# Kernel tuning notes

Measured on AMD Instinct MI355X. Metric: run time of the kernel, lower is better.

The kernel has to match this reference:

```python
import jax, jax.numpy as jnp
import numpy as np

NUM_CLASSES = 3
DICE_W, FOCAL_W, CONTR_W = 1.0, 1.0, 0.1
GAMMA, ALPHA = 2.0, 0.25
TEMP = 0.1
SCALE_WEIGHTS = (1.0, 0.8, 0.6)
SMOOTH = 1e-5


def setup_inputs() -> dict:
    key = jax.random.key(0)
    ks = jax.random.split(key, 7)
    return {
        "pred_maps": jax.random.normal(ks[0], (2, 3, 128, 128, 128), jnp.float32),
        "target": jax.random.randint(ks[1], (2, 128, 128, 128), 0, 3, jnp.int64),
        "fmap0": jax.random.normal(ks[2], (2, 48, 16, 16, 16), jnp.float32),
        "fmap1": jax.random.normal(ks[3], (2, 48, 8, 8, 8), jnp.float32),
        "fmap2": jax.random.normal(ks[4], (2, 48, 4, 4, 4), jnp.float32),
        "logits": jax.random.normal(ks[5], (2, 3), jnp.float32),
        "labels": jax.random.randint(ks[6], (2, 3), 0, 2, jnp.int32),
    }


def _dice_loss(pred, target):
    p = jax.nn.softmax(pred, axis=1)                      # [B,C,H,W,D]
    t = jnp.where(target == -1, 0, target)
    oh = jax.nn.one_hot(t, NUM_CLASSES, axis=1, dtype=p.dtype)  # [B,C,H,W,D]
    inter = (p * oh).sum((2, 3, 4))                       # [B,C]
    union = p.sum((2, 3, 4)) + oh.sum((2, 3, 4))
    dice = (2.0 * inter + SMOOTH) / (union + SMOOTH)      # [B,C]
    return 1.0 - dice[:, 1:].mean()                       # exclude background


def _focal_loss(logits, labels):
    pt = jax.nn.sigmoid(logits)
    pt = jnp.where(labels == 1, pt, 1.0 - pt)
    return (-ALPHA * (1.0 - pt) ** GAMMA * jnp.log(pt + 1e-6)).mean()


def _pair_loss(E, wa, wb, offdiag, positive):
    # E: [B,N,N] exp(sim/T); wa, wb: [B,N] class indicator weights
    W = wa[:, :, None] * wb[:, None, :]
    if offdiag is not None:
        W = W * offdiag
    cnt = W.sum((1, 2))
    mean = (E * W).sum((1, 2)) / jnp.maximum(cnt, 1.0)
    val = -jnp.log(mean + 1e-6) if positive else jnp.log1p(mean)
    return jnp.where(cnt > 0, val, 0.0)                   # [B]


def _scale_loss(feat, mask):
    B, C = feat.shape[:2]
    f = feat.reshape(B, C, -1)                            # [B,C,N]
    norm = jnp.sqrt((f * f).sum(1, keepdims=True))
    f = f / jnp.maximum(norm, 1e-12)                      # F.normalize(dim=1)
    m = mask.reshape(B, -1)                               # [B,N]
    E = jnp.exp(jnp.einsum('bcn,bcm->bnm', f, f) / TEMP)  # [B,N,N]
    N = m.shape[1]
    off = 1.0 - jnp.eye(N, dtype=f.dtype)
    w0 = (m == 0).astype(f.dtype)
    w1 = (m == 1).astype(f.dtype)
    w2 = (m == 2).astype(f.dtype)
    loss = _pair_loss(E, w1, w1, off, True)               # htx positive
    loss += _pair_loss(E, w2, w2, off, True)              # mh positive
    loss += _pair_loss(E, w1, w2, None, False)            # htx vs mh
    loss += _pair_loss(E, w0, w1, None, False)            # bg vs htx
    loss += _pair_loss(E, w0, w2, None, False)            # bg vs mh
    return loss.mean()                                    # batch_loss / B


def _contrastive_loss(fmaps, target):
    H = target.shape[1]
    total = 0.0
    for feat, w in zip(fmaps, SCALE_WEIGHTS):
        s = H // feat.shape[2]                            # exact nearest-downsample stride
        mask = target[:, ::s, ::s, ::s]
        total += w * _scale_loss(feat, mask)
    return total


def reference(pred_maps, target, fmap0, fmap1, fmap2, logits, labels):
    dice = _dice_loss(pred_maps, target)
    focal = _focal_loss(logits, labels)
    contr = _contrastive_loss((fmap0, fmap1, fmap2), target)
    total = DICE_W * dice + FOCAL_W * focal + CONTR_W * contr
    return (total, dice, focal, contr)
```

## Files before the change

kernel.cpp:

```cpp
#include <hip/hip_runtime.h>
#include <math.h>

#define VOX (128*128*128)
#define NCH 48

typedef _Float16 half8 __attribute__((ext_vector_type(8)));
typedef float floatx4 __attribute__((ext_vector_type(4)));

__device__ __forceinline__ float waveSum(float v) {
#pragma unroll
    for (int off = 32; off > 0; off >>= 1) v += __shfl_down(v, off, 64);
    return v;
}


__device__ __forceinline__ int elem_class(const int* __restrict__ target,
                                          int scale, int b, int n) {
    const int d = (scale == 0) ? 16 : (scale == 1) ? 8 : 4;
    const int s = 128 / d;
    int i3 = n % d, i2 = (n / d) % d, i1 = n / (d * d);
    return target[(size_t)b * VOX + (size_t)(i1 * s) * 16384 + (i2 * s) * 128 + (i3 * s)];
}

__global__ __launch_bounds__(256) void count_kernel(const int* __restrict__ target,
                                                    int* __restrict__ count_stage) {
    const int scale = blockIdx.y, b = blockIdx.z, z = scale * 2 + b, bx = blockIdx.x;
    const int N    = (scale == 0) ? 4096 : (scale == 1) ? 512 : 64;
    const int Npad = (scale == 0) ? 4096 : (scale == 1) ? 512 : 128;
    const int n = bx * 256 + threadIdx.x;
    int myK = -1;
    if (n < N)          myK = elem_class(target, scale, b, n);
    else if (n < Npad)  myK = 3;

    __shared__ int wc[4][4];
    const int lane = threadIdx.x & 63, w = threadIdx.x >> 6;
#pragma unroll
    for (int k = 0; k < 4; k++) {
        unsigned long long mb = __ballot(myK == k);
        if (lane == 0) wc[w][k] = (int)__popcll(mb);
    }
    __syncthreads();
    if (threadIdx.x < 4)
        count_stage[(z * 16 + bx) * 4 + threadIdx.x] =
            wc[0][threadIdx.x] + wc[1][threadIdx.x] + wc[2][threadIdx.x] + wc[3][threadIdx.x];
}

__global__ __launch_bounds__(256) void norm_scatter(const float* __restrict__ f0in,
                                                    const float* __restrict__ f1in,
                                                    const float* __restrict__ f2in,
                                                    const int* __restrict__ target,
                                                    _Float16* __restrict__ Fh0,
                                                    _Float16* __restrict__ Fh1,
                                                    _Float16* __restrict__ Fh2,
                                                    const int* __restrict__ count_stage) {
    const int scale = blockIdx.y, b = blockIdx.z, z = scale * 2 + b, bx = blockIdx.x;
    const int N    = (scale == 0) ? 4096 : (scale == 1) ? 512 : 64;
    const int Npad = (scale == 0) ? 4096 : (scale == 1) ? 512 : 128;
    if (bx * 256 >= Npad) return;
    const int tid = threadIdx.x, lane = tid & 63, w = tid >> 6;
    const int n = bx * 256 + tid;

    __shared__ int cs[64];
    __shared__ int wcls[4][4];
    if (tid < 64) cs[tid] = count_stage[z * 64 + tid];

    int myK = -1;
    if (n < N)         myK = elem_class(target, scale, b, n);
    else if (n < Npad) myK = 3;

    const unsigned long long below = (lane == 63) ? ~0ull >> 1 : (1ull << lane) - 1ull;
    int laneRank = 0;
#pragma unroll
    for (int k = 0; k < 4; k++) {
        unsigned long long mb = __ballot(myK == k);
        if (lane == 0) wcls[w][k] = (int)__popcll(mb);
        if (myK == k) laneRank = (int)__popcll(mb & below);
    }
    __syncthreads();
    if (myK < 0) return;

    int total[4];
#pragma unroll
    for (int k = 0; k < 4; k++) {
        int s = 0;
        for (int r = 0; r < 16; r++) s += cs[r * 4 + k];
        total[k] = s;
    }
    int dest = laneRank;
    for (int k = 0; k < myK; k++) dest += total[k];
    for (int r = 0; r < bx; r++) dest += cs[r * 4 + myK];
    for (int ww = 0; ww < w; ww++) dest += wcls[ww][myK];

    float v[NCH];
    float inv = 0.0f;
    if (n < N) {
        const float* fi = ((scale == 0) ? f0in : (scale == 1) ? f1in : f2in)
                          + (size_t)b * NCH * N + n;
        float ss = 0.0f;
#pragma unroll
        for (int c = 0; c < NCH; c++) { v[c] = fi[(size_t)c * N]; ss += v[c] * v[c]; }
        inv = 1.0f / fmaxf(sqrtf(ss), 1e-12f);
    } else {
#pragma unroll
        for (int c = 0; c < NCH; c++) v[c] = 0.0f;
    }
    _Float16* fo = ((scale == 0) ? Fh0 : (scale == 1) ? Fh1 : Fh2)
                   + (size_t)b * Npad * 64 + (size_t)dest * 64;
#pragma unroll
    for (int g = 0; g < 8; g++) {
        half8 h;
#pragma unroll
        for (int e = 0; e < 8; e++) {
            int c = g * 8 + e;
            h[e] = (c < NCH) ? (_Float16)(v[c] * inv) : (_Float16)0.0f;
        }
        *(half8*)(fo + g * 8) = h;
    }
}

__global__ __launch_bounds__(256) void dice_pair(const float* __restrict__ pred,
                                                 const int* __restrict__ target,
                                                 const _Float16* __restrict__ Fh0,
                                                 const _Float16* __restrict__ Fh1,
                                                 const _Float16* __restrict__ Fh2,
                                                 const int* __restrict__ count_stage,
                                                 float* __restrict__ dice_stage,
                                                 float* __restrict__ pair_stage) {
    const int bid = blockIdx.x;
    const int tid = threadIdx.x, lane = tid & 63, w = tid >> 6;
    __shared__ float red[4][6];

    if (bid >= 550) {
        const int local = bid - 550;
        const int b = local >> 9, bx = local & 511;
        const float4* p0 = (const float4*)(pred + (size_t)b * 3 * VOX);
        const float4* p1 = (const float4*)(pred + (size_t)b * 3 * VOX + VOX);
        const float4* p2 = (const float4*)(pred + (size_t)b * 3 * VOX + 2 * VOX);
        const int4*   tg = (const int4*)(target + (size_t)b * VOX);

        float vals[6] = {0, 0, 0, 0, 0, 0};
        const int V4 = VOX / 4;
        for (int v = bx * 256 + tid; v < V4; v += 512 * 256) {
            float4 a = p0[v], bq = p1[v], cq = p2[v];
            int4 t = tg[v];
            float xs[4][3] = {{a.x, bq.x, cq.x}, {a.y, bq.y, cq.y},
                              {a.z, bq.z, cq.z}, {a.w, bq.w, cq.w}};
            int ts[4] = {t.x, t.y, t.z, t.w};
#pragma unroll
            for (int e = 0; e < 4; e++) {
                float e0 = __expf(xs[e][0]), e1 = __expf(xs[e][1]), e2 = __expf(xs[e][2]);
                float inv = 1.0f / (e0 + e1 + e2);
                float q1 = e1 * inv, q2 = e2 * inv;
                vals[2] += q1;
                vals[3] += q2;
                int tt = ts[e];
                vals[0] += (tt == 1) ? q1 : 0.0f;
                vals[1] += (tt == 2) ? q2 : 0.0f;
                vals[4] += (tt == 1) ? 1.0f : 0.0f;
                vals[5] += (tt == 2) ? 1.0f : 0.0f;
            }
        }
#pragma unroll
        for (int k = 0; k < 6; k++) {
            float s = waveSum(vals[k]);
            if (lane == 0) red[w][k] = s;
        }
        __syncthreads();
        if (tid < 6) {
            float s = red[0][tid] + red[1][tid] + red[2][tid] + red[3][tid];
            dice_stage[(size_t)local * 8 + tid] = s;
        }
        return;
    }

    int z, t0, nt, tstep;
    if (bid < 528)      { z = bid / 264; t0 = bid % 264; nt = 2; tstep = 264; }
    else if (bid < 548) { int i = bid - 528; z = 2 + i / 10; t0 = i % 10; nt = 1; tstep = 0; }
    else                { z = 4 + (bid - 548); t0 = 0; nt = 1; tstep = 0; }

    const int scale = z >> 1, b = z & 1;
    const int Npad = (scale == 0) ? 4096 : (scale == 1) ? 512 : 128;
    const _Float16* F = ((scale == 0) ? Fh0 : (scale == 1) ? Fh1 : Fh2)
                        + (size_t)b * Npad * 64;
    int B1 = 0, B2 = 0, B3 = 0;
    for (int r = 0; r < 16; r++) {
        B1 += count_stage[(z * 16 + r) * 4 + 0];
        B2 += count_stage[(z * 16 + r) * 4 + 1];
        B3 += count_stage[(z * 16 + r) * 4 + 2];
    }
    B2 += B1; B3 += B2;

    const int wi = w >> 1, wj = w & 1;
    const int m = lane & 15, q = lane >> 4;

    float s[5] = {0, 0, 0, 0, 0};

    for (int it = 0; it < nt; it++) {
        int t = t0 + it * tstep;
        int by = (int)((sqrtf(8.0f * (float)t + 1.0f) - 1.0f) * 0.5f);
        while ((by + 1) * (by + 2) / 2 <= t) by++;
        while (by * (by + 1) / 2 > t) by--;
        int bx = t - by * (by + 1) / 2;

        const int ib = bx * 128 + wi * 64, jb = by * 128 + wj * 64;

        const bool diag = (ib == jb);
        const bool below = (ib > jb);
        int ciL = (ib >= B1) + (ib >= B2) + (ib >= B3);
        int ciH = (ib + 63 >= B1) + (ib + 63 >= B2) + (ib + 63 >= B3);
        int cjL = (jb >= B1) + (jb >= B2) + (jb >= B3);
        int cjH = (jb + 63 >= B1) + (jb + 63 >= B2) + (jb + 63 >= B3);
        const bool pure = (ciL == ciH) && (cjL == cjH) && !diag;
        int bucket = -1;
        float mult = 1.0f;
        if (pure) {
            int ci = ciL, cj = cjL;
            if (ci == 1 && cj == 1) { bucket = 0; mult = 2.0f; }
            else if (ci == 2 && cj == 2) { bucket = 1; mult = 2.0f; }
            else if (ci == 1 && cj == 2) bucket = 2;
            else if (ci == 0 && cj == 1) bucket = 3;
            else if (ci == 0 && cj == 2) bucket = 4;
        }
        if (below || (pure && bucket < 0)) continue;

        const _Float16* Ai = F + (size_t)(ib + m) * 64 + q * 8;
        const _Float16* Bj = F + (size_t)(jb + m) * 64 + q * 8;

        floatx4 acc_[4][4] = {};
#pragma unroll
        for (int k = 0; k < 2; k++) {
            half8 aF[4], bF[4];
#pragma unroll
            for (int t4 = 0; t4 < 4; t4++) {
                aF[t4] = *(const half8*)(Ai + t4 * 16 * 64 + k * 32);
                bF[t4] = *(const half8*)(Bj + t4 * 16 * 64 + k * 32);
            }
#pragma unroll
            for (int ti = 0; ti < 4; ti++)
#pragma unroll
                for (int tj = 0; tj < 4; tj++)
                    acc_[ti][tj] = __builtin_amdgcn_mfma_f32_16x16x32_f16(
                        aF[ti], bF[tj], acc_[ti][tj], 0, 0, 0);
        }

        if (pure) {
            float ps[4] = {0, 0, 0, 0};
#pragma unroll
            for (int ti = 0; ti < 4; ti++)
#pragma unroll
                for (int tj = 0; tj < 4; tj++)
#pragma unroll
                    for (int r = 0; r < 4; r++)
                        ps[r] += __expf(acc_[ti][tj][r] * 10.0f);
            s[bucket] += ((ps[0] + ps[1]) + (ps[2] + ps[3])) * mult;
        } else {
#pragma unroll
            for (int ti = 0; ti < 4; ti++) {
#pragma unroll
                for (int tj = 0; tj < 4; tj++) {
#pragma unroll
                    for (int r = 0; r < 4; r++) {
                        int gi = ib + ti * 16 + q * 4 + r;
                        int gj = jb + tj * 16 + m;
                        float e = __expf(acc_[ti][tj][r] * 10.0f);
                        bool ok = !diag || (gi < gj);
                        int ci = (gi >= B1) + (gi >= B2) + (gi >= B3);
                        int cj = (gj >= B1) + (gj >= B2) + (gj >= B3);
                        s[0] += (ok && ci == 1 && cj == 1) ? e + e : 0.0f;
                        s[1] += (ok && ci == 2 && cj == 2) ? e + e : 0.0f;
                        s[2] += (ok && ci == 1 && cj == 2) ? e : 0.0f;
                        s[3] += (ok && ci == 0 && cj == 1) ? e : 0.0f;
                        s[4] += (ok && ci == 0 && cj == 2) ? e : 0.0f;
                    }
                }
            }
        }
    }

#pragma unroll
    for (int k = 0; k < 5; k++) {
        float r = waveSum(s[k]);
        if (lane == 0) red[w][k] = r;
    }
    __syncthreads();
    if (tid < 5) {
        float r = red[0][tid] + red[1][tid] + red[2][tid] + red[3][tid];
        pair_stage[(size_t)bid * 8 + tid] = r;
    }
}

__global__ __launch_bounds__(512) void reduce_finalize(const float* __restrict__ dice_stage,
                                                       const int* __restrict__ count_stage,
                                                       const float* __restrict__ pair_stage,
                                                       const float* __restrict__ logits,
                                                       const int* __restrict__ labels,
                                                       float* __restrict__ out) {
    __shared__ float D[2][6], S[6][5], CNT[6][4];
    const int tid = threadIdx.x, w = tid >> 6, lane = tid & 63;

    if (w < 2) {
        float v[6] = {0, 0, 0, 0, 0, 0};
#pragma unroll
        for (int i = 0; i < 8; i++) {
            const float* row = dice_stage + (size_t)(w * 512 + i * 64 + lane) * 8;
#pragma unroll
            for (int k = 0; k < 6; k++) v[k] += row[k];
        }
#pragma unroll
        for (int k = 0; k < 6; k++) {
            float r = waveSum(v[k]);
            if (lane == 0) D[w][k] = r;
        }
    } else {
        int z = w - 2;
        int start = (z == 0) ? 0 : (z == 1) ? 264 : (z == 2) ? 528
                    : (z == 3) ? 538 : (z == 4) ? 548 : 549;
        int n = (z < 2) ? 264 : (z < 4) ? 10 : 1;
        float v[5] = {0, 0, 0, 0, 0};
        for (int i = lane; i < n; i += 64) {
            const float* row = pair_stage + (size_t)(start + i) * 8;
#pragma unroll
            for (int k = 0; k < 5; k++) v[k] += row[k];
        }
#pragma unroll
        for (int k = 0; k < 5; k++) {
            float r = waveSum(v[k]);
            if (lane == 0) S[z][k] = r;
        }
        float c[4] = {0, 0, 0, 0};
        if (lane < 16) {
#pragma unroll
            for (int k = 0; k < 4; k++)
                c[k] = (float)count_stage[(z * 16 + lane) * 4 + k];
        }
#pragma unroll
        for (int k = 0; k < 4; k++) {
            float r = waveSum(c[k]);
            if (lane == 0) CNT[z][k] = r;
        }
    }
    __syncthreads();
    if (tid != 0) return;

    float dsum = 0.0f;
    for (int b = 0; b < 2; b++)
        for (int c = 0; c < 2; c++)
            dsum += (2.0f * D[b][c] + 1e-5f) / (D[b][2 + c] + D[b][4 + c] + 1e-5f);
    float dice = 1.0f - dsum * 0.25f;

    float fsum = 0.0f;
    for (int i = 0; i < 6; i++) {
        float x = logits[i];
        float pt = 1.0f / (1.0f + __expf(-x));
        if (labels[i] != 1) pt = 1.0f - pt;
        fsum += -0.25f * (1.0f - pt) * (1.0f - pt) * logf(pt + 1e-6f);
    }
    float focal = fsum * (1.0f / 6.0f);

    const float sw[3] = {1.0f, 0.8f, 0.6f};
    float contr = 0.0f;
    for (int sc = 0; sc < 3; sc++) {
        float bsum = 0.0f;
        for (int b = 0; b < 2; b++) {
            int z = sc * 2 + b;
            float S11 = S[z][0], S22 = S[z][1], S12 = S[z][2],
                  S01 = S[z][3], S02 = S[z][4];
            float c0 = CNT[z][0], c1 = CNT[z][1], c2 = CNT[z][2];
            float l = 0.0f, c, mean;
            c = c1 * c1 - c1; mean = S11 / fmaxf(c, 1.0f);
            l += (c > 0.0f) ? -logf(mean + 1e-6f) : 0.0f;
            c = c2 * c2 - c2; mean = S22 / fmaxf(c, 1.0f);
            l += (c > 0.0f) ? -logf(mean + 1e-6f) : 0.0f;
            c = c1 * c2; mean = S12 / fmaxf(c, 1.0f);
            l += (c > 0.0f) ? log1pf(mean) : 0.0f;
            c = c0 * c1; mean = S01 / fmaxf(c, 1.0f);
            l += (c > 0.0f) ? log1pf(mean) : 0.0f;
            c = c0 * c2; mean = S02 / fmaxf(c, 1.0f);
            l += (c > 0.0f) ? log1pf(mean) : 0.0f;
            bsum += l;
        }
        contr += sw[sc] * bsum * 0.5f;
    }
    float total = dice + focal + 0.1f * contr;
    out[0] = total;
    out[1] = dice;
    out[2] = focal;
    out[3] = contr;
}

extern "C" void kernel_launch(void* const* d_in, const int* in_sizes, int n_in,
                              void* d_out, int out_size, void* d_ws, size_t ws_size,
                              hipStream_t stream) {
    const float* pred   = (const float*)d_in[0];
    const int*   target = (const int*)d_in[1];
    const float* f0     = (const float*)d_in[2];
    const float* f1     = (const float*)d_in[3];
    const float* f2     = (const float*)d_in[4];
    const float* logits = (const float*)d_in[5];
    const int*   labels = (const int*)d_in[6];
    float* out = (float*)d_out;

    char* ws = (char*)d_ws;
    int*   count_stage = (int*)ws;
    float* dice_stage  = (float*)(ws + 4096);
    float* pair_stage  = (float*)(ws + 36864);
    _Float16* Fh0 = (_Float16*)(ws + 131072);
    _Float16* Fh1 = (_Float16*)(ws + 1179648);
    _Float16* Fh2 = (_Float16*)(ws + 1310720);

    count_kernel<<<dim3(16, 3, 2), dim3(256), 0, stream>>>(target, count_stage);
    norm_scatter<<<dim3(16, 3, 2), dim3(256), 0, stream>>>(f0, f1, f2, target,
                                                           Fh0, Fh1, Fh2, count_stage);
    dice_pair<<<dim3(1574), dim3(256), 0, stream>>>(pred, target, Fh0, Fh1, Fh2,
                                                    count_stage, dice_stage, pair_stage);
    reduce_finalize<<<dim3(1), dim3(512), 0, stream>>>(dice_stage, count_stage,
                                                       pair_stage, logits, labels, out);
}
```

Baseline: 130.1 us.

## Fuse count into scatter and finalize into dice_pair via last-block ticket

Removes the separate count kernel by having each norm_scatter block recompute the per-chunk class counts of its scale and batch redundantly. It also removes the final reduce kernel: dice_pair blocks take an atomic ticket, and the last block to arrive runs the global reduction and loss formula. The aim is to cut the launch and dependency gaps between four small kernels down to two. The cost is duplicated target gathers, atomic and fence overhead, and a serial tail in the last block.

Measured after the change: 287.8 us. 121% more time.

```diff
diff --git a/kernel.cpp b/kernel.cpp
--- a/kernel.cpp
+++ b/kernel.cpp
@@ -11,6 +11,10 @@
 #pragma unroll
     for (int off = 32; off > 0; off >>= 1) v += __shfl_down(v, off, 64);
     return v;
+}
+
+__device__ __forceinline__ float aload(const float* p) {
+    return __hip_atomic_load(p, __ATOMIC_RELAXED, __HIP_MEMORY_SCOPE_AGENT);
 }
 
 
@@ -20,29 +24,6 @@
     const int s = 128 / d;
     int i3 = n % d, i2 = (n / d) % d, i1 = n / (d * d);
     return target[(size_t)b * VOX + (size_t)(i1 * s) * 16384 + (i2 * s) * 128 + (i3 * s)];
-}
-
-__global__ __launch_bounds__(256) void count_kernel(const int* __restrict__ target,
-                                                    int* __restrict__ count_stage) {
-    const int scale = blockIdx.y, b = blockIdx.z, z = scale * 2 + b, bx = blockIdx.x;
-    const int N    = (scale == 0) ? 4096 : (scale == 1) ? 512 : 64;
-    const int Npad = (scale == 0) ? 4096 : (scale == 1) ? 512 : 128;
-    const int n = bx * 256 + threadIdx.x;
-    int myK = -1;
-    if (n < N)          myK = elem_class(target, scale, b, n);
-    else if (n < Npad)  myK = 3;
-
-    __shared__ int wc[4][4];
-    const int lane = threadIdx.x & 63, w = threadIdx.x >> 6;
-#pragma unroll
-    for (int k = 0; k < 4; k++) {
-        unsigned long long mb = __ballot(myK == k);
-        if (lane == 0) wc[w][k] = (int)__popcll(mb);
-    }
-    __syncthreads();
-    if (threadIdx.x < 4)
-        count_stage[(z * 16 + bx) * 4 + threadIdx.x] =
-            wc[0][threadIdx.x] + wc[1][threadIdx.x] + wc[2][threadIdx.x] + wc[3][threadIdx.x];
 }
 
 __global__ __launch_bounds__(256) void norm_scatter(const float* __restrict__ f0in,
@@ -52,45 +33,55 @@
                                                     _Float16* __restrict__ Fh0,
                                                     _Float16* __restrict__ Fh1,
                                                     _Float16* __restrict__ Fh2,
-                                                    const int* __restrict__ count_stage) {
+                                                    int* __restrict__ cnt,
+                                                    int* __restrict__ ticket) {
     const int scale = blockIdx.y, b = blockIdx.z, z = scale * 2 + b, bx = blockIdx.x;
     const int N    = (scale == 0) ? 4096 : (scale == 1) ? 512 : 64;
     const int Npad = (scale == 0) ? 4096 : (scale == 1) ? 512 : 128;
-    if (bx * 256 >= Npad) return;
+    const int nCh  = (Npad + 255) / 256;
     const int tid = threadIdx.x, lane = tid & 63, w = tid >> 6;
+
+    if (scale == 0 && b == 0 && bx == 0 && tid == 0) *ticket = 0;
+    if (bx >= nCh) return;
+
+    __shared__ int cw[16][4][4];
+    int myK = -1, laneRank = 0;
+    const unsigned long long below = (1ull << lane) - 1ull;
+
+    for (int r = 0; r < nCh; r++) {
+        int nn = r * 256 + tid, k = -1;
+        if (nn < N)         k = elem_class(target, scale, b, nn);
+        else if (nn < Npad) k = 3;
+        if (r == bx) myK = k;
+#pragma unroll
+        for (int kk = 0; kk < 4; kk++) {
+            unsigned long long mb = __ballot(k == kk);
+            if (lane == 0) cw[r][w][kk] = (int)__popcll(mb);
+            if (r == bx && k == kk) laneRank = (int)__popcll(mb & below);
+        }
+    }
+    __syncthreads();
+
+    if (bx == 0 && tid < 4) {
+        int s = 0;
+        for (int r = 0; r < nCh; r++)
+            for (int ww = 0; ww < 4; ww++) s += cw[r][ww][tid];
+        cnt[z * 4 + tid] = s;
+    }
+    if (myK < 0) return;
+
+    int dest = laneRank;
+    for (int k = 0; k < myK; k++) {
+        int s = 0;
+        for (int r = 0; r < nCh; r++)
+            for (int ww = 0; ww < 4; ww++) s += cw[r][ww][k];
+        dest += s;
+    }
+    for (int r = 0; r < bx; r++)
+        for (int ww = 0; ww < 4; ww++) dest += cw[r][ww][myK];
+    for (int ww = 0; ww < w; ww++) dest += cw[bx][ww][myK];
+
     const int n = bx * 256 + tid;
-
-    __shared__ int cs[64];
-    __shared__ int wcls[4][4];
-    if (tid < 64) cs[tid] = count_stage[z * 64 + tid];
-
-    int myK = -1;
-    if (n < N)         myK = elem_class(target, scale, b, n);
-    else if (n < Npad) myK = 3;
-
-    const unsigned long long below = (lane == 63) ? ~0ull >> 1 : (1ull << lane) - 1ull;
-    int laneRank = 0;
-#pragma unroll
-    for (int k = 0; k < 4; k++) {
-        unsigned long long mb = __ballot(myK == k);
-        if (lane == 0) wcls[w][k] = (int)__popcll(mb);
-        if (myK == k) laneRank = (int)__popcll(mb & below);
-    }
-    __syncthreads();
-    if (myK < 0) return;
-
-    int total[4];
-#pragma unroll
-    for (int k = 0; k < 4; k++) {
-        int s = 0;
-        for (int r = 0; r < 16; r++) s += cs[r * 4 + k];
-        total[k] = s;
-    }
-    int dest = laneRank;
-    for (int k = 0; k < myK; k++) dest += total[k];
-    for (int r = 0; r < bx; r++) dest += cs[r * 4 + myK];
-    for (int ww = 0; ww < w; ww++) dest += wcls[ww][myK];
-
     float v[NCH];
     float inv = 0.0f;
     if (n < N) {
@@ -123,9 +114,13 @@
                                                  const _Float16* __restrict__ Fh0,
                                                  const _Float16* __restrict__ Fh1,
                                                  const _Float16* __restrict__ Fh2,
-                                                 const int* __restrict__ count_stage,
+                                                 const int* __restrict__ cnt,
+                                                 int* __restrict__ ticket,
                                                  float* __restrict__ dice_stage,
-                                                 float* __restrict__ pair_stage) {
+                                                 float* __restrict__ pair_stage,
+                                                 const float* __restrict__ logits,
+                                                 const int* __restrict__ labels,
+                                                 float* __restrict__ out) {
     const int bid = blockIdx.x;
     const int tid = threadIdx.x, lane = tid & 63, w = tid >> 6;
     __shared__ float red[4][6];
@@ -170,141 +165,134 @@
             float s = red[0][tid] + red[1][tid] + red[2][tid] + red[3][tid];
             dice_stage[(size_t)local * 8 + tid] = s;
         }
-        return;
-    }
-
-    int z, t0, nt, tstep;
-    if (bid < 528)      { z = bid / 264; t0 = bid % 264; nt = 2; tstep = 264; }
-    else if (bid < 548) { int i = bid - 528; z = 2 + i / 10; t0 = i % 10; nt = 1; tstep = 0; }
-    else                { z = 4 + (bid - 548); t0 = 0; nt = 1; tstep = 0; }
-
-    const int scale = z >> 1, b = z & 1;
-    const int Npad = (scale == 0) ? 4096 : (scale == 1) ? 512 : 128;
-    const _Float16* F = ((scale == 0) ? Fh0 : (scale == 1) ? Fh1 : Fh2)
-                        + (size_t)b * Npad * 64;
-    int B1 = 0, B2 = 0, B3 = 0;
-    for (int r = 0; r < 16; r++) {
-        B1 += count_stage[(z * 16 + r) * 4 + 0];
-        B2 += count_stage[(z * 16 + r) * 4 + 1];
-        B3 += count_stage[(z * 16 + r) * 4 + 2];
-    }
-    B2 += B1; B3 += B2;
-
-    const int wi = w >> 1, wj = w & 1;
-    const int m = lane & 15, q = lane >> 4;
-
-    float s[5] = {0, 0, 0, 0, 0};
-
-    for (int it = 0; it < nt; it++) {
-        int t = t0 + it * tstep;
-        int by = (int)((sqrtf(8.0f * (float)t + 1.0f) - 1.0f) * 0.5f);
-        while ((by + 1) * (by + 2) / 2 <= t) by++;
-        while (by * (by + 1) / 2 > t) by--;
-        int bx = t - by * (by + 1) / 2;
-
-        const int ib = bx * 128 + wi * 64, jb = by * 128 + wj * 64;
-
-        const bool diag = (ib == jb);
-        const bool below = (ib > jb);
-        int ciL = (ib >= B1) + (ib >= B2) + (ib >= B3);
-        int ciH = (ib + 63 >= B1) + (ib + 63 >= B2) + (ib + 63 >= B3);
-        int cjL = (jb >= B1) + (jb >= B2) + (jb >= B3);
-        int cjH = (jb + 63 >= B1) + (jb + 63 >= B2) + (jb + 63 >= B3);
-        const bool pure = (ciL == ciH) && (cjL == cjH) && !diag;
-        int bucket = -1;
-        float mult = 1.0f;
-        if (pure) {
-            int ci = ciL, cj = cjL;
-            if (ci == 1 && cj == 1) { bucket = 0; mult = 2.0f; }
-            else if (ci == 2 && cj == 2) { bucket = 1; mult = 2.0f; }
-            else if (ci == 1 && cj == 2) bucket = 2;
-            else if (ci == 0 && cj == 1) bucket = 3;
-            else if (ci == 0 && cj == 2) bucket = 4;
-        }
-        if (below || (pure && bucket < 0)) continue;
-
-        const _Float16* Ai = F + (size_t)(ib + m) * 64 + q * 8;
-        const _Float16* Bj = F + (size_t)(jb + m) * 64 + q * 8;
-
-        floatx4 acc_[4][4] = {};
-#pragma unroll
-        for (int k = 0; k < 2; k++) {
-            half8 aF[4], bF[4];
-#pragma unroll
-            for (int t4 = 0; t4 < 4; t4++) {
-                aF[t4] = *(const half8*)(Ai + t4 * 16 * 64 + k * 32);
-                bF[t4] = *(const half8*)(Bj + t4 * 16 * 64 + k * 32);
-            }
-#pragma unroll
-            for (int ti = 0; ti < 4; ti++)
-#pragma unroll
-                for (int tj = 0; tj < 4; tj++)
-                    acc_[ti][tj] = __builtin_amdgcn_mfma_f32_16x16x32_f16(
-                        aF[ti], bF[tj], acc_[ti][tj], 0, 0, 0);
-        }
-
-        if (pure) {
-            float ps[4] = {0, 0, 0, 0};
-#pragma unroll
-            for (int ti = 0; ti < 4; ti++)
-#pragma unroll
-                for (int tj = 0; tj < 4; tj++)
-#pragma unroll
-                    for (int r = 0; r < 4; r++)
-                        ps[r] += __expf(acc_[ti][tj][r] * 10.0f);
-            s[bucket] += ((ps[0] + ps[1]) + (ps[2] + ps[3])) * mult;
-        } else {
-#pragma unroll
-            for (int ti = 0; ti < 4; ti++) {
-#pragma unroll
-                for (int tj = 0; tj < 4; tj++) {
-#pragma unroll
-                    for (int r = 0; r < 4; r++) {
-                        int gi = ib + ti * 16 + q * 4 + r;
-                        int gj = jb + tj * 16 + m;
-                        float e = __expf(acc_[ti][tj][r] * 10.0f);
-                        bool ok = !diag || (gi < gj);
-                        int ci = (gi >= B1) + (gi >= B2) + (gi >= B3);
-                        int cj = (gj >= B1) + (gj >= B2) + (gj >= B3);
-                        s[0] += (ok && ci == 1 && cj == 1) ? e + e : 0.0f;
-                        s[1] += (ok && ci == 2 && cj == 2) ? e + e : 0.0f;
-                        s[2] += (ok && ci == 1 && cj == 2) ? e : 0.0f;
-                        s[3] += (ok && ci == 0 && cj == 1) ? e : 0.0f;
-                        s[4] += (ok && ci == 0 && cj == 2) ? e : 0.0f;
+    } else {
+        int z, t0, nt, tstep;
+        if (bid < 528)      { z = bid / 264; t0 = bid % 264; nt = 2; tstep = 264; }
+        else if (bid < 548) { int i = bid - 528; z = 2 + i / 10; t0 = i % 10; nt = 1; tstep = 0; }
+        else                { z = 4 + (bid - 548); t0 = 0; nt = 1; tstep = 0; }
+
+        const int scale = z >> 1, b = z & 1;
+        const int Npad = (scale == 0) ? 4096 : (scale == 1) ? 512 : 128;
+        const _Float16* F = ((scale == 0) ? Fh0 : (scale == 1) ? Fh1 : Fh2)
+                            + (size_t)b * Npad * 64;
+        const int B1 = cnt[z * 4 + 0];
+        const int B2 = B1 + cnt[z * 4 + 1];
+        const int B3 = B2 + cnt[z * 4 + 2];
+
+        const int wi = w >> 1, wj = w & 1;
+        const int m = lane & 15, q = lane >> 4;
+
+        float s[5] = {0, 0, 0, 0, 0};
+
+        for (int it = 0; it < nt; it++) {
+            int t = t0 + it * tstep;
+            int by = (int)((sqrtf(8.0f * (float)t + 1.0f) - 1.0f) * 0.5f);
+            while ((by + 1) * (by + 2) / 2 <= t) by++;
+            while (by * (by + 1) / 2 > t) by--;
+            int bx = t - by * (by + 1) / 2;
+
+            const int ib = bx * 128 + wi * 64, jb = by * 128 + wj * 64;
+
+            const bool diag = (ib == jb);
+            const bool belowq = (ib > jb);
+            int ciL = (ib >= B1) + (ib >= B2) + (ib >= B3);
+            int ciH = (ib + 63 >= B1) + (ib + 63 >= B2) + (ib + 63 >= B3);
+            int cjL = (jb >= B1) + (jb >= B2) + (jb >= B3);
+            int cjH = (jb + 63 >= B1) + (jb + 63 >= B2) + (jb + 63 >= B3);
+            const bool pure = (ciL == ciH) && (cjL == cjH) && !diag;
+            int bucket = -1;
+            float mult = 1.0f;
+            if (pure) {
+                int ci = ciL, cj = cjL;
+                if (ci == 1 && cj == 1) { bucket = 0; mult = 2.0f; }
+                else if (ci == 2 && cj == 2) { bucket = 1; mult = 2.0f; }
+                else if (ci == 1 && cj == 2) bucket = 2;
+                else if (ci == 0 && cj == 1) bucket = 3;
+                else if (ci == 0 && cj == 2) bucket = 4;
+            }
+            if (belowq || (pure && bucket < 0)) continue;
+
+            const _Float16* Ai = F + (size_t)(ib + m) * 64 + q * 8;
+            const _Float16* Bj = F + (size_t)(jb + m) * 64 + q * 8;
+
+            floatx4 acc_[4][4] = {};
+#pragma unroll
+            for (int k = 0; k < 2; k++) {
+                half8 aF[4], bF[4];
+#pragma unroll
+                for (int t4 = 0; t4 < 4; t4++) {
+                    aF[t4] = *(const half8*)(Ai + t4 * 16 * 64 + k * 32);
+                    bF[t4] = *(const half8*)(Bj + t4 * 16 * 64 + k * 32);
+                }
+#pragma unroll
+                for (int ti = 0; ti < 4; ti++)
+#pragma unroll
+                    for (int tj = 0; tj < 4; tj++)
+                        acc_[ti][tj] = __builtin_amdgcn_mfma_f32_16x16x32_f16(
+                            aF[ti], bF[tj], acc_[ti][tj], 0, 0, 0);
+            }
+
+            if (pure) {
+                float ps[4] = {0, 0, 0, 0};
+#pragma unroll
+                for (int ti = 0; ti < 4; ti++)
+#pragma unroll
+                    for (int tj = 0; tj < 4; tj++)
+#pragma unroll
+                        for (int r = 0; r < 4; r++)
+                            ps[r] += __expf(acc_[ti][tj][r] * 10.0f);
+                s[bucket] += ((ps[0] + ps[1]) + (ps[2] + ps[3])) * mult;
+            } else {
+#pragma unroll
+                for (int ti = 0; ti < 4; ti++) {
+#pragma unroll
+                    for (int tj = 0; tj < 4; tj++) {
+#pragma unroll
+                        for (int r = 0; r < 4; r++) {
+                            int gi = ib + ti * 16 + q * 4 + r;
+                            int gj = jb + tj * 16 + m;
+                            float e = __expf(acc_[ti][tj][r] * 10.0f);
+                            bool ok = !diag || (gi < gj);
+                            int ci = (gi >= B1) + (gi >= B2) + (gi >= B3);
+                            int cj = (gj >= B1) + (gj >= B2) + (gj >= B3);
+                            s[0] += (ok && ci == 1 && cj == 1) ? e + e : 0.0f;
+                            s[1] += (ok && ci == 2 && cj == 2) ? e + e : 0.0f;
+                            s[2] += (ok && ci == 1 && cj == 2) ? e : 0.0f;
+                            s[3] += (ok && ci == 0 && cj == 1) ? e : 0.0f;
+                            s[4] += (ok && ci == 0 && cj == 2) ? e : 0.0f;
+                        }
                     }
                 }
             }
         }
-    }
-
-#pragma unroll
-    for (int k = 0; k < 5; k++) {
-        float r = waveSum(s[k]);
-        if (lane == 0) red[w][k] = r;
-    }
+
+#pragma unroll
+        for (int k = 0; k < 5; k++) {
+            float r = waveSum(s[k]);
+            if (lane == 0) red[w][k] = r;
+        }
+        __syncthreads();
+        if (tid < 5) {
+            float r = red[0][tid] + red[1][tid] + red[2][tid] + red[3][tid];
+            pair_stage[(size_t)bid * 8 + tid] = r;
+        }
+    }
+
+    __threadfence();
+    __shared__ int isLast;
+    if (tid == 0) isLast = (atomicAdd(ticket, 1) == 1573);
     __syncthreads();
-    if (tid < 5) {
-        float r = red[0][tid] + red[1][tid] + red[2][tid] + red[3][tid];
-        pair_stage[(size_t)bid * 8 + tid] = r;
-    }
-}
-
-__global__ __launch_bounds__(512) void reduce_finalize(const float* __restrict__ dice_stage,
-                                                       const int* __restrict__ count_stage,
-                                                       const float* __restrict__ pair_stage,
-                                                       const float* __restrict__ logits,
-                                                       const int* __restrict__ labels,
-                                                       float* __restrict__ out) {
-    __shared__ float D[2][6], S[6][5], CNT[6][4];
-    const int tid = threadIdx.x, w = tid >> 6, lane = tid & 63;
-
+    if (!isLast) return;
+    __threadfence();
+
+    __shared__ float D[2][6], S[6][5];
     if (w < 2) {
         float v[6] = {0, 0, 0, 0, 0, 0};
 #pragma unroll
         for (int i = 0; i < 8; i++) {
             const float* row = dice_stage + (size_t)(w * 512 + i * 64 + lane) * 8;
 #pragma unroll
-            for (int k = 0; k < 6; k++) v[k] += row[k];
+            for (int k = 0; k < 6; k++) v[k] += aload(row + k);
         }
 #pragma unroll
         for (int k = 0; k < 6; k++) {
@@ -312,31 +300,37 @@
             if (lane == 0) D[w][k] = r;
         }
     } else {
-        int z = w - 2;
-        int start = (z == 0) ? 0 : (z == 1) ? 264 : (z == 2) ? 528
-                    : (z == 3) ? 538 : (z == 4) ? 548 : 549;
-        int n = (z < 2) ? 264 : (z < 4) ? 10 : 1;
-        float v[5] = {0, 0, 0, 0, 0};
-        for (int i = lane; i < n; i += 64) {
-            const float* row = pair_stage + (size_t)(start + i) * 8;
-#pragma unroll
-            for (int k = 0; k < 5; k++) v[k] += row[k];
-        }
-#pragma unroll
-        for (int k = 0; k < 5; k++) {
-            float r = waveSum(v[k]);
-            if (lane == 0) S[z][k] = r;
-        }
-        float c[4] = {0, 0, 0, 0};
-        if (lane < 16) {
-#pragma unroll
-            for (int k = 0; k < 4; k++)
-                c[k] = (float)count_stage[(z * 16 + lane) * 4 + k];
-        }
-#pragma unroll
-        for (int k = 0; k < 4; k++) {
-            float r = waveSum(c[k]);
-            if (lane == 0) CNT[z][k] = r;
+        int zz = w - 2;
+        {
+            float v[5] = {0, 0, 0, 0, 0};
+            for (int i = lane; i < 264; i += 64) {
+                const float* row = pair_stage + (size_t)(zz * 264 + i) * 8;
+#pragma unroll
+                for (int k = 0; k < 5; k++) v[k] += aload(row + k);
+            }
+#pragma unroll
+            for (int k = 0; k < 5; k++) {
+                float r = waveSum(v[k]);
+                if (lane == 0) S[zz][k] = r;
+            }
+        }
+        {
+            float v[5] = {0, 0, 0, 0, 0};
+            if (lane < 10) {
+                const float* row = pair_stage + (size_t)(528 + zz * 10 + lane) * 8;
+#pragma unroll
+                for (int k = 0; k < 5; k++) v[k] = aload(row + k);
+            }
+#pragma unroll
+            for (int k = 0; k < 5; k++) {
+                float r = waveSum(v[k]);
+                if (lane == 0) S[2 + zz][k] = r;
+            }
+        }
+        if (lane == 0) {
+            const float* row = pair_stage + (size_t)(548 + zz) * 8;
+#pragma unroll
+            for (int k = 0; k < 5; k++) S[4 + zz][k] = aload(row + k);
         }
     }
     __syncthreads();
@@ -365,7 +359,8 @@
             int z = sc * 2 + b;
             float S11 = S[z][0], S22 = S[z][1], S12 = S[z][2],
                   S01 = S[z][3], S02 = S[z][4];
-            float c0 = CNT[z][0], c1 = CNT[z][1], c2 = CNT[z][2];
+            float c0 = (float)cnt[z * 4 + 0], c1 = (float)cnt[z * 4 + 1],
+                  c2 = (float)cnt[z * 4 + 2];
             float l = 0.0f, c, mean;
             c = c1 * c1 - c1; mean = S11 / fmaxf(c, 1.0f);
             l += (c > 0.0f) ? -logf(mean + 1e-6f) : 0.0f;
@@ -401,18 +396,17 @@
     float* out = (float*)d_out;
 
     char* ws = (char*)d_ws;
-    int*   count_stage = (int*)ws;
-    float* dice_stage  = (float*)(ws + 4096);
-    float* pair_stage  = (float*)(ws + 36864);
+    int*   cnt        = (int*)ws;
+    int*   ticket     = (int*)(ws + 2048);
+    float* dice_stage = (float*)(ws + 4096);
+    float* pair_stage = (float*)(ws + 36864);
     _Float16* Fh0 = (_Float16*)(ws + 131072);
     _Float16* Fh1 = (_Float16*)(ws + 1179648);
     _Float16* Fh2 = (_Float16*)(ws + 1310720);
 
-    count_kernel<<<dim3(16, 3, 2), dim3(256), 0, stream>>>(target, count_stage);
     norm_scatter<<<dim3(16, 3, 2), dim3(256), 0, stream>>>(f0, f1, f2, target,
-                                                           Fh0, Fh1, Fh2, count_stage);
+                                                           Fh0, Fh1, Fh2, cnt, ticket);
     dice_pair<<<dim3(1574), dim3(256), 0, stream>>>(pred, target, Fh0, Fh1, Fh2,
-                                                    count_stage, dice_stage, pair_stage);
-    reduce_finalize<<<dim3(1), dim3(512), 0, stream>>>(dice_stage, count_stage,
-                                                       pair_stage, logits, labels, out);
-}
+                                                    cnt, ticket, dice_stage, pair_stage,
+                                                    logits, labels, out);
+}
```
